# Performance work log

Measured on AMD Instinct MI355X. Metric: run time of the kernel, lower is better.

Reference implementation:

```python
import jax, jax.numpy as jnp
import numpy as np

EPS = 1e-5


def _lstm(x, W_ih, W_hh, b_ih, b_hh):
    # x: [B, T, in]; torch LSTM gate order i, f, g, o. Returns (last h, last c).
    def step(carry, xt):
        h, c = carry
        z = xt @ W_ih.T + h @ W_hh.T + (b_ih + b_hh)  # [B, 4H]
        i, f, g, o = jnp.split(z, 4, axis=-1)
        c = jax.nn.sigmoid(f) * c + jax.nn.sigmoid(i) * jnp.tanh(g)
        h = jax.nn.sigmoid(o) * jnp.tanh(c)
        return (h, c), None
    h0 = jnp.zeros((x.shape[0], W_hh.shape[1]), x.dtype)
    (h, c), _ = jax.lax.scan(step, (h0, h0), jnp.swapaxes(x, 0, 1))
    return h, c


def _bn_train(x, g, b):
    # BatchNorm1d in training mode: batch stats, biased variance.
    m = x.mean(axis=0)
    v = x.var(axis=0)
    return g * (x - m) * jax.lax.rsqrt(v + EPS) + b


def _forward(agent_traj, neighbours, aW_ih, aW_hh, ab_ih, ab_hh,
             nW_ih, nW_hh, nb_ih, nb_hh, dW_ih, dW_hh, db_ih, db_hh,
             pW, pb, rW, rb, m1W, m1b, g1, be1, m2W, m2b, g2, be2,
             i1W, i1b, ig1, ib1, i2W, i2b, ig2, ib2, segment_ids):
    B = agent_traj.shape[0]
    # relative distance: neighbour last position - owning agent's last position
    rel = neighbours[:, -1, :] - agent_traj[segment_ids, -1, :]          # [N, 2]
    agent_h, agent_c = _lstm(agent_traj, aW_ih, aW_hh, ab_ih, ab_hh)     # [B, 64]
    neigh_h, _ = _lstm(neighbours, nW_ih, nW_hh, nb_ih, nb_hh)           # [N, 64]
    rel_emb = rel @ rW.T + rb                                            # [N, 64]
    x = jnp.concatenate([neigh_h, rel_emb], axis=1)                      # [N, 128]
    x = _bn_train(jax.nn.relu(x @ m1W.T + m1b), g1, be1)                 # [N, 512]
    x = _bn_train(jax.nn.relu(x @ m2W.T + m2b), g2, be2)                 # [N, 1024]
    # per-sample max pooling over each sample's neighbours (zeros if none)
    pooled = jax.ops.segment_max(x, segment_ids, num_segments=B)         # [B, 1024]
    counts = jax.ops.segment_sum(jnp.ones((x.shape[0],), x.dtype), segment_ids, num_segments=B)
    pooled = jnp.where(counts[:, None] > 0, pooled, jnp.zeros((), x.dtype))
    d = jnp.concatenate([pooled, agent_h], axis=1)                       # [B, 1088]
    d = _bn_train(jax.nn.relu(d @ i1W.T + i1b), ig1, ib1)                # [B, 1024]
    d = _bn_train(jax.nn.relu(d @ i2W.T + i2b), ig2, ib2)                # [B, 64]

    def dec_step(carry, _):
        h, c = carry
        z = h @ dW_ih.T + h @ dW_hh.T + (db_ih + db_hh)
        i, f, g, o = jnp.split(z, 4, axis=-1)
        c = jax.nn.sigmoid(f) * c + jax.nn.sigmoid(i) * jnp.tanh(g)
        h = jax.nn.sigmoid(o) * jnp.tanh(c)
        return (h, c), h
    _, hs = jax.lax.scan(dec_step, (d, agent_c), None, length=30)        # [30, B, 64]
    pred = jnp.einsum('tbh,oh->bto', hs, pW) + pb                        # [B, 30, 2]
    return pred


def setup_inputs() -> dict:
    B, T, N, Tn, H = 2048, 20, 32768, 20, 64
    key = jax.random.key(0)
    ki = iter(jax.random.split(key, 40))
    def rn(shape, s=0.1):
        return jax.random.normal(next(ki), shape, dtype=jnp.float32) * s
    inp = dict(
        agent_traj=rn((B, T, 2), 1.0),
        neighbours=rn((N, Tn, 2), 1.0),
        aW_ih=rn((4 * H, 2)), aW_hh=rn((4 * H, H)), ab_ih=rn((4 * H,)), ab_hh=rn((4 * H,)),
        nW_ih=rn((4 * H, 2)), nW_hh=rn((4 * H, H)), nb_ih=rn((4 * H,)), nb_hh=rn((4 * H,)),
        dW_ih=rn((4 * H, H)), dW_hh=rn((4 * H, H)), db_ih=rn((4 * H,)), db_hh=rn((4 * H,)),
        pW=rn((2, H)), pb=rn((2,)),
        rW=rn((H, 2)), rb=rn((H,)),
        m1W=rn((512, 128)), m1b=rn((512,)),
        g1=jnp.ones((512,), jnp.float32), be1=jnp.zeros((512,), jnp.float32),
        m2W=rn((1024, 512)), m2b=rn((1024,)),
        g2=jnp.ones((1024,), jnp.float32), be2=jnp.zeros((1024,), jnp.float32),
        i1W=rn((1024, 1088)), i1b=rn((1024,)),
        ig1=jnp.ones((1024,), jnp.float32), ib1=jnp.zeros((1024,), jnp.float32),
        i2W=rn((H, 1024)), i2b=rn((H,)),
        ig2=jnp.ones((H,), jnp.float32), ib2=jnp.zeros((H,), jnp.float32),
        segment_ids=jnp.sort(jax.random.randint(next(ki), (N,), 0, B)).astype(jnp.int32),
    )
    return inp


def reference(agent_traj, neighbours, aW_ih, aW_hh, ab_ih, ab_hh,
              nW_ih, nW_hh, nb_ih, nb_hh, dW_ih, dW_hh, db_ih, db_hh,
              pW, pb, rW, rb, m1W, m1b, g1, be1, m2W, m2b, g2, be2,
              i1W, i1b, ig1, ib1, i2W, i2b, ig2, ib2, segment_ids):
    return _forward(agent_traj, neighbours, aW_ih, aW_hh, ab_ih, ab_hh,
                    nW_ih, nW_hh, nb_ih, nb_hh, dW_ih, dW_hh, db_ih, db_hh,
                    pW, pb, rW, rb, m1W, m1b, g1, be1, m2W, m2b, g2, be2,
                    i1W, i1b, ig1, ib1, i2W, i2b, ig2, ib2, segment_ids)
```

## Files before the change

kernel.cpp:

```cpp
#include <hip/hip_runtime.h>

#define EPS_BN 1e-5f

typedef __attribute__((ext_vector_type(8))) short short8;
typedef __attribute__((ext_vector_type(4))) float f32x4;

__device__ __forceinline__ float fast_rcp(float x) { return __builtin_amdgcn_rcpf(x); }
__device__ __forceinline__ float sigmoid_f(float x) { return fast_rcp(1.0f + __expf(-x)); }
__device__ __forceinline__ float tanh_f(float x) { return 1.0f - 2.0f * fast_rcp(__expf(2.0f * x) + 1.0f); }

__device__ __forceinline__ unsigned short f2bf(float f) {
    unsigned u = __float_as_uint(f);
    u += 0x7FFFu + ((u >> 16) & 1u);
    return (unsigned short)(u >> 16);
}
__device__ __forceinline__ unsigned pk_bf(float a, float b) {
    return (unsigned)f2bf(a) | ((unsigned)f2bf(b) << 16);
}
__device__ __forceinline__ float bf_hi(float f) {
    return __uint_as_float((unsigned)f2bf(f) << 16);
}
__device__ __forceinline__ float bf2f(unsigned short u) {
    return __uint_as_float((unsigned)u << 16);
}

union AFrag { short e[8]; short8 v; };
union BFrag { uint4 u; short8 v; };

__global__ __launch_bounds__(256, 2) void lstm_mfma(
    const float* __restrict__ xA,
    const float* __restrict__ aW_ih, const float* __restrict__ aW_hh,
    const float* __restrict__ ab_ih, const float* __restrict__ ab_hh,
    float* __restrict__ agent_h, float* __restrict__ agent_c,
    const float* __restrict__ xN,
    const float* __restrict__ nW_ih, const float* __restrict__ nW_hh,
    const float* __restrict__ nb_ih, const float* __restrict__ nb_hh,
    float* __restrict__ neigh_h,
    int nAgentBlk, int T)
{
    __shared__ unsigned h_ex[2][2][32 * 52];

    const bool isA = (blockIdx.x < (unsigned)nAgentBlk);
    const long blk = isA ? blockIdx.x : blockIdx.x - nAgentBlk;
    const float* __restrict__ x     = isA ? xA   : xN;
    const float* __restrict__ W_ih  = isA ? aW_ih : nW_ih;
    const float* __restrict__ W_hh  = isA ? aW_hh : nW_hh;
    const float* __restrict__ b_ih  = isA ? ab_ih : nb_ih;
    const float* __restrict__ b_hh  = isA ? ab_hh : nb_hh;
    float* __restrict__ h_out = isA ? agent_h : neigh_h;
    float* __restrict__ c_out = isA ? agent_c : nullptr;

    const int tid  = threadIdx.x;
    const int w    = tid >> 6;
    const int lane = tid & 63;
    const int s    = lane & 15;
    const int q    = lane >> 4;

    short8 ahi[4][3], alo[4][3];
#pragma unroll
    for (int gt = 0; gt < 4; ++gt) {
        const int n = gt * 64 + w * 16 + s;
#pragma unroll
        for (int kc = 0; kc < 2; ++kc) {
            const float* src = &W_hh[n * 64 + kc * 32 + q * 8];
            float4 v0 = *(const float4*)src;
            float4 v1 = *(const float4*)(src + 4);
            float v[8] = {v0.x, v0.y, v0.z, v0.w, v1.x, v1.y, v1.z, v1.w};
            AFrag a, b;
#pragma unroll
            for (int j = 0; j < 8; ++j) {
                a.e[j] = (short)f2bf(v[j]);
                b.e[j] = (short)f2bf(v[j] - bf_hi(v[j]));
            }
            ahi[gt][kc] = a.v;
            alo[gt][kc] = b.v;
        }
        AFrag a2, b2;
#pragma unroll
        for (int j = 0; j < 8; ++j) { a2.e[j] = 0; b2.e[j] = 0; }
        if (q == 0) {
            const float wi0 = W_ih[n * 2 + 0];
            const float wi1 = W_ih[n * 2 + 1];
            const float bs  = b_ih[n] + b_hh[n];
            a2.e[0] = (short)f2bf(wi0); b2.e[0] = (short)f2bf(wi0 - bf_hi(wi0));
            a2.e[1] = (short)f2bf(wi1); b2.e[1] = (short)f2bf(wi1 - bf_hi(wi1));
            a2.e[2] = (short)f2bf(bs);  b2.e[2] = (short)f2bf(bs  - bf_hi(bs));
        }
        ahi[gt][2] = a2.v;
        alo[gt][2] = b2.v;
    }

    for (int i = tid; i < 2 * 2 * 32 * 52; i += 256) (&h_ex[0][0][0])[i] = 0u;
    __syncthreads();
    if (tid < 32) {
        h_ex[0][0][tid * 52 + 33] = pk_bf(1.0f, 0.0f);
        h_ex[1][0][tid * 52 + 33] = pk_bf(1.0f, 0.0f);
        float2 xv = *(const float2*)&x[(blk * 32 + tid) * (long)(T * 2)];
        h_ex[0][0][tid * 52 + 32] = pk_bf(xv.x, xv.y);
        h_ex[0][1][tid * 52 + 32] = pk_bf(xv.x - bf_hi(xv.x), xv.y - bf_hi(xv.y));
    }
    __syncthreads();

    float creg[2][4] = {{0.f, 0.f, 0.f, 0.f}, {0.f, 0.f, 0.f, 0.f}};

    for (int t = 0; t < T; ++t) {
        const int rb = t & 1, wb = rb ^ 1;
        BFrag bhi[2][3], blo[2][3];
#pragma unroll
        for (int g = 0; g < 2; ++g)
#pragma unroll
        for (int kc = 0; kc < 3; ++kc) {
            const int off = (g * 16 + s) * 52 + kc * 16 + (q >> 1) * 8 + (q & 1) * 4;
            bhi[g][kc].u = *(const uint4*)&h_ex[rb][0][off];
            blo[g][kc].u = *(const uint4*)&h_ex[rb][1][off];
        }

        f32x4 acc[4][2];
#pragma unroll
        for (int gt = 0; gt < 4; ++gt) { acc[gt][0] = (f32x4)0.f; acc[gt][1] = (f32x4)0.f; }

#pragma unroll
        for (int kc = 0; kc < 3; ++kc) {
#pragma unroll
            for (int g = 0; g < 2; ++g) {
                const short8 bh = bhi[g][kc].v;
                const short8 bl = blo[g][kc].v;
#pragma unroll
                for (int gt = 0; gt < 4; ++gt) {
                    f32x4 a = acc[gt][g];
                    a = __builtin_amdgcn_mfma_f32_16x16x32_bf16(ahi[gt][kc], bh, a, 0, 0, 0);
                    a = __builtin_amdgcn_mfma_f32_16x16x32_bf16(ahi[gt][kc], bl, a, 0, 0, 0);
                    a = __builtin_amdgcn_mfma_f32_16x16x32_bf16(alo[gt][kc], bh, a, 0, 0, 0);
                    acc[gt][g] = a;
                }
            }
        }

#pragma unroll
        for (int g = 0; g < 2; ++g) {
            float hval[4];
#pragma unroll
            for (int r = 0; r < 4; ++r) {
                const float ei = __expf(-acc[0][g][r]);
                const float eg = __expf(2.0f * acc[2][g][r]);
                const float it = (eg - 1.0f) * fast_rcp((1.0f + ei) * (eg + 1.0f));
                const float sf = fast_rcp(1.0f + __expf(-acc[1][g][r]));
                const float c  = fmaf(sf, creg[g][r], it);
                creg[g][r] = c;
                const float eo = __expf(-acc[3][g][r]);
                const float ec = __expf(2.0f * c);
                hval[r] = (ec - 1.0f) * fast_rcp((1.0f + eo) * (ec + 1.0f));
            }
            {
                const int w0 = (g * 16 + s) * 52 + w * 8 + q * 2;
                h_ex[wb][0][w0]     = pk_bf(hval[0], hval[1]);
                h_ex[wb][0][w0 + 1] = pk_bf(hval[2], hval[3]);
                h_ex[wb][1][w0]     = pk_bf(hval[0] - bf_hi(hval[0]), hval[1] - bf_hi(hval[1]));
                h_ex[wb][1][w0 + 1] = pk_bf(hval[2] - bf_hi(hval[2]), hval[3] - bf_hi(hval[3]));
            }
            if (t == T - 1) {
                const long seq = blk * 32 + g * 16 + s;
                const int j0 = w * 16 + q * 4;
                *(float4*)&h_out[seq * 64 + j0] = make_float4(hval[0], hval[1], hval[2], hval[3]);
                if (c_out)
                    *(float4*)&c_out[seq * 64 + j0] =
                        make_float4(creg[g][0], creg[g][1], creg[g][2], creg[g][3]);
            }
        }
        if (tid < 32 && t + 1 < T) {
            float2 xv = *(const float2*)&x[(blk * 32 + tid) * (long)(T * 2) + (t + 1) * 2];
            h_ex[wb][0][tid * 52 + 32] = pk_bf(xv.x, xv.y);
            h_ex[wb][1][tid * 52 + 32] = pk_bf(xv.x - bf_hi(xv.x), xv.y - bf_hi(xv.y));
        }
        __syncthreads();
    }
}

__global__ __launch_bounds__(256) void build_x0(
    const float* __restrict__ neigh_h, const float* __restrict__ neighbours,
    const float* __restrict__ agent_traj, const int* __restrict__ seg,
    const float* __restrict__ rW, const float* __restrict__ rb,
    unsigned short* __restrict__ x0hi, unsigned short* __restrict__ x0lo, int T)
{
    const long n = (long)blockIdx.x * 2 + (threadIdx.x >> 7);
    const int j = threadIdx.x & 127;
    float v;
    if (j < 64) {
        v = neigh_h[n*64 + j];
    } else {
        const int o = j - 64;
        const int sid = seg[n];
        const float ra = neighbours[n*(long)(T*2) + (T-1)*2 + 0] - agent_traj[(long)sid*(T*2) + (T-1)*2 + 0];
        const float rbv= neighbours[n*(long)(T*2) + (T-1)*2 + 1] - agent_traj[(long)sid*(T*2) + (T-1)*2 + 1];
        v = fmaf(rW[o*2+0], ra, fmaf(rW[o*2+1], rbv, rb[o]));
    }
    x0hi[n*128 + j] = f2bf(v);
    x0lo[n*128 + j] = f2bf(v - bf_hi(v));
}

__global__ __launch_bounds__(64) void prep_wfrag(
    const float* __restrict__ W, const float* __restrict__ sc, int K,
    unsigned short* __restrict__ Whi, unsigned short* __restrict__ Wlo)
{
    const int nKc = K >> 5;
    const int blk = blockIdx.x;
    const int ti = blk / nKc, kc = blk - ti * nKc;
    const int l = threadIdx.x;
    const int n = ti * 16 + (l & 15);
    const int k0 = kc * 32 + (l >> 4) * 8;
    const long ob = ((long)blk * 64 + l) * 8;
#pragma unroll
    for (int j = 0; j < 8; ++j) {
        float v = W[(long)n * K + k0 + j];
        if (sc) v *= sc[k0 + j];
        Whi[ob + j] = f2bf(v);
        Wlo[ob + j] = f2bf(v - bf_hi(v));
    }
}

__global__ __launch_bounds__(64) void prep_bias(
    const float* __restrict__ W, const float* __restrict__ sh,
    const float* __restrict__ b, int K, float* __restrict__ bout)
{
    const int n = blockIdx.x;
    const int l = threadIdx.x;
    float s = 0.f;
    if (sh)
        for (int k = l; k < K; k += 64) s += sh[k] * W[(long)n * K + k];
#pragma unroll
    for (int m = 32; m >= 1; m >>= 1) s += __shfl_xor(s, m, 64);
    if (l == 0) bout[n] = b[n] + s;
}

__global__ __launch_bounds__(256, 2) void gemm_split(
    const unsigned short* __restrict__ Ahi,
    const unsigned short* __restrict__ Alo,
    const unsigned short* __restrict__ Whi,
    const unsigned short* __restrict__ Wlo,
    const float* __restrict__ bias,
    float* __restrict__ Yf,
    unsigned short* __restrict__ Yhi,
    unsigned short* __restrict__ Ylo,
    float* __restrict__ accum,
    const int* __restrict__ segp,
    float* __restrict__ poolmax,
    int M, int K, int O)
{
    __shared__ unsigned short As[2][2][128 * 56];
    __shared__ int segl[128];
    const int t = threadIdx.x;
    const int lane = t & 63;
    const int w = t >> 6;
    const int wm = w & 1, wn = w >> 1;

    const int nx = gridDim.x;
    const int flat = blockIdx.y * nx + blockIdx.x;
    const int grp = flat / (8 * nx);
    const int loc = flat - grp * (8 * nx);
    const int m0 = (grp * 8 + (loc & 7)) * 128;
    const int n0 = (loc >> 3) * 128;
    const int nKc = K >> 5;

    f32x4 acc[4][4];
#pragma unroll
    for (int mt = 0; mt < 4; ++mt)
#pragma unroll
    for (int nt = 0; nt < 4; ++nt) acc[mt][nt] = (f32x4)0.f;

    const long aoff = (long)(m0 + (t >> 1)) * K + (t & 1) * 16;
    const unsigned short* aph = Ahi + aoff;
    const unsigned short* apl = Alo + aoff;
    const int so = (t >> 1) * 56 + (t & 1) * 16;
    const int arow = wm * 64 + (lane & 15);
    const int acol = (lane >> 4) * 8;
    const long bt0 = (long)((n0 >> 4) + wn * 4);

    uint4 rah0, rah1, ral0, ral1;
    auto loadAreg = [&](int kc) {
        rah0 = *(const uint4*)(aph + kc * 32);
        rah1 = *(const uint4*)(aph + kc * 32 + 8);
        ral0 = *(const uint4*)(apl + kc * 32);
        ral1 = *(const uint4*)(apl + kc * 32 + 8);
    };
    auto storeAs = [&](int buf) {
        *(uint4*)&As[buf][0][so] = rah0; *(uint4*)&As[buf][0][so + 8] = rah1;
        *(uint4*)&As[buf][1][so] = ral0; *(uint4*)&As[buf][1][so + 8] = ral1;
    };
    auto loadB = [&](BFrag* bh, BFrag* bl, int kc) {
#pragma unroll
        for (int nt = 0; nt < 4; ++nt) {
            const long fb = ((bt0 + nt) * nKc + kc) * 512 + lane * 8;
            bh[nt].u = *(const uint4*)(Whi + fb);
            bl[nt].u = *(const uint4*)(Wlo + fb);
        }
    };
    auto compute = [&](int buf, BFrag* bh, BFrag* bl) {
        BFrag afh[4], afl[4];
#pragma unroll
        for (int mt = 0; mt < 4; ++mt) {
            afh[mt].u = *(const uint4*)&As[buf][0][(arow + mt * 16) * 56 + acol];
            afl[mt].u = *(const uint4*)&As[buf][1][(arow + mt * 16) * 56 + acol];
        }
#pragma unroll
        for (int nt = 0; nt < 4; ++nt)
#pragma unroll
        for (int mt = 0; mt < 4; ++mt) {
            f32x4 a = acc[mt][nt];
            a = __builtin_amdgcn_mfma_f32_16x16x32_bf16(afh[mt].v, bh[nt].v, a, 0, 0, 0);
            a = __builtin_amdgcn_mfma_f32_16x16x32_bf16(afh[mt].v, bl[nt].v, a, 0, 0, 0);
            a = __builtin_amdgcn_mfma_f32_16x16x32_bf16(afl[mt].v, bh[nt].v, a, 0, 0, 0);
            acc[mt][nt] = a;
        }
    };

    BFrag bh0[4], bl0[4], bh1[4], bl1[4];
    loadAreg(0);
    loadB(bh0, bl0, 0);
    storeAs(0);
    __syncthreads();
    for (int kc = 0; kc < nKc; kc += 2) {
        loadAreg(kc + 1);
        loadB(bh1, bl1, kc + 1);
        compute(0, bh0, bl0);
        storeAs(1);
        __syncthreads();
        if (kc + 2 < nKc) {
            loadAreg(kc + 2);
            loadB(bh0, bl0, kc + 2);
        }
        compute(1, bh1, bl1);
        if (kc + 2 < nKc) {
            storeAs(0);
            __syncthreads();
        }
    }

    int sid0 = 0, span = 0;
    bool useLds = false;
    float* pool = nullptr;
    if (segp) {
        __syncthreads();
        if (t < 128) segl[t] = segp[m0 + t];
        __syncthreads();
        sid0 = segl[0];
        span = segl[127] - sid0 + 1;
        pool = (float*)&As[0][0][0];
        useLds = (span <= 104);
        if (useLds) {
            for (int i = t; i < span * 132; i += 256) pool[i] = 0.f;
            __syncthreads();
        }
    }

    const int cn = lane & 15, cq = lane >> 4;
#pragma unroll
    for (int nt = 0; nt < 4; ++nt) {
        const int cl = wn * 64 + nt * 16 + cn;
        const int n = n0 + cl;
        const float bs = bias[n];
        float s = 0.f, ssq = 0.f;
#pragma unroll
        for (int mt = 0; mt < 4; ++mt) {
            const int mb = wm * 64 + mt * 16 + cq * 4;
            float vmax = 0.f; int sid = -1;
#pragma unroll
            for (int r = 0; r < 4; ++r) {
                const float v = fmaxf(acc[mt][nt][r] + bs, 0.f);
                s += v; ssq += v * v;
                if (segp) {
                    const int sr = segl[mb + r];
                    if (r == 0) { vmax = v; sid = sr; }
                    else if (sr == sid) { vmax = fmaxf(vmax, v); }
                    else {
                        if (vmax > 0.f) {
                            if (useLds)
                                atomicMax((int*)&pool[(sid - sid0) * 132 + cl], __float_as_int(vmax));
                            else
                                atomicMax((int*)&poolmax[(long)sid * O + n], __float_as_int(vmax));
                        }
                        sid = sr; vmax = v;
                    }
                } else if (Yf) {
                    Yf[(long)(m0 + mb + r) * O + n] = v;
                } else {
                    const long idx = (long)(m0 + mb + r) * O + n;
                    Yhi[idx] = f2bf(v);
                    Ylo[idx] = f2bf(v - bf_hi(v));
                }
            }
            if (segp && vmax > 0.f) {
                if (useLds)
                    atomicMax((int*)&pool[(sid - sid0) * 132 + cl], __float_as_int(vmax));
                else
                    atomicMax((int*)&poolmax[(long)sid * O + n], __float_as_int(vmax));
            }
        }
        if (accum) {
            s   += __shfl_xor(s, 16, 64);   ssq += __shfl_xor(ssq, 16, 64);
            s   += __shfl_xor(s, 32, 64);   ssq += __shfl_xor(ssq, 32, 64);
            if (cq == 0) {
                atomicAdd(&accum[n], s);
                atomicAdd(&accum[O + n], ssq);
            }
        }
    }

    if (segp && useLds) {
        __syncthreads();
        for (int e = t; e < span * 128; e += 256) {
            const int sl = e >> 7, c = e & 127;
            const float v = pool[sl * 132 + c];
            const long gi = (long)(sid0 + sl) * O + (n0 + c);
            if (sl == 0 || sl == span - 1) {
                if (v > 0.f) atomicMax((int*)&poolmax[gi], __float_as_int(v));
            } else {
                poolmax[gi] = v;
            }
        }
    }
}

__global__ __launch_bounds__(256) void colstats(
    const float* __restrict__ Y, int M, int O, int chunkRows,
    float* __restrict__ accum)
{
    const int c = blockIdx.x * 64 + (threadIdx.x & 63);
    const int rgrp = threadIdx.x >> 6;
    const int r0 = blockIdx.y * chunkRows;
    int rend = r0 + chunkRows; if (rend > M) rend = M;
    float s = 0.f, ss = 0.f;
    for (int r = r0 + rgrp; r < rend; r += 4) {
        const float v = Y[(long)r*O + c];
        s += v; ss += v*v;
    }
    __shared__ float l1[256], l2[256];
    l1[threadIdx.x] = s; l2[threadIdx.x] = ss;
    __syncthreads();
    if (threadIdx.x < 64) {
        const int c2 = blockIdx.x * 64 + threadIdx.x;
        s  = l1[threadIdx.x] + l1[threadIdx.x+64] + l1[threadIdx.x+128] + l1[threadIdx.x+192];
        ss = l2[threadIdx.x] + l2[threadIdx.x+64] + l2[threadIdx.x+128] + l2[threadIdx.x+192];
        atomicAdd(&accum[c2], s);
        atomicAdd(&accum[O + c2], ss);
    }
}

__global__ __launch_bounds__(256) void bn_finalize(
    const float* __restrict__ accum, const float* __restrict__ g,
    const float* __restrict__ be, int O, float invM,
    float* __restrict__ scale, float* __restrict__ shift)
{
    const int o = blockIdx.x * 256 + threadIdx.x;
    if (o < O) {
        const float mean = accum[o] * invM;
        const float var  = accum[O + o] * invM - mean * mean;
        const float sc   = g[o] * rsqrtf(var + EPS_BN);
        scale[o] = sc;
        shift[o] = be[o] - mean * sc;
    }
}

__global__ __launch_bounds__(256) void build_d0(
    const float* __restrict__ poolraw, const float* __restrict__ agent_h,
    const int* __restrict__ seg, int N,
    const float* __restrict__ sc2, const float* __restrict__ sh2,
    unsigned short* __restrict__ d0hi, unsigned short* __restrict__ d0lo)
{
    const int b = blockIdx.x;
    int l = 0, h = N;
    while (l < h) { const int mid = (l + h) >> 1; if (seg[mid] < b) l = mid + 1; else h = mid; }
    const bool nonempty = (l < N) && (seg[l] == b);
    for (int c = threadIdx.x; c < 1088; c += 256) {
        float v;
        if (c < 1024) {
            v = nonempty ? fmaf(sc2[c], poolraw[(long)b*1024 + c], sh2[c]) : 0.f;
        } else {
            v = agent_h[(long)b*64 + (c - 1024)];
        }
        d0hi[(long)b*1088 + c] = f2bf(v);
        d0lo[(long)b*1088 + c] = f2bf(v - bf_hi(v));
    }
}

__global__ __launch_bounds__(256) void gemm_i2_part(
    const float* __restrict__ A,
    const float* __restrict__ W,
    const float* __restrict__ ascale, const float* __restrict__ ashift,
    float* __restrict__ part, int M, int K, int kchunk)
{
    __shared__ float As[16][132];
    __shared__ float Bs[16][68];
    const int t = threadIdx.x;
    const int m0 = blockIdx.x * 128;
    const int ks = blockIdx.y;
    const int kbeg = ks * kchunk;
    const int kend = kbeg + kchunk;
    const int tm = (t & 15) * 8;
    const int tn = (t >> 4) * 4;
    const int ar = t >> 1;
    const int ac = (t & 1) * 8;
    const int br = t >> 2;
    const int bc = (t & 3) * 4;

    float acc[8][4];
#pragma unroll
    for (int i = 0; i < 8; ++i)
#pragma unroll
    for (int j = 0; j < 4; ++j) acc[i][j] = 0.f;

    for (int k0 = kbeg; k0 < kend; k0 += 16) {
        float4 a0 = *(const float4*)&A[(long)(m0+ar)*K + k0 + ac];
        float4 a1 = *(const float4*)&A[(long)(m0+ar)*K + k0 + ac + 4];
        float4 s0 = *(const float4*)&ascale[k0 + ac];
        float4 s1 = *(const float4*)&ascale[k0 + ac + 4];
        float4 h0 = *(const float4*)&ashift[k0 + ac];
        float4 h1 = *(const float4*)&ashift[k0 + ac + 4];
        a0.x = fmaf(a0.x, s0.x, h0.x); a0.y = fmaf(a0.y, s0.y, h0.y);
        a0.z = fmaf(a0.z, s0.z, h0.z); a0.w = fmaf(a0.w, s0.w, h0.w);
        a1.x = fmaf(a1.x, s1.x, h1.x); a1.y = fmaf(a1.y, s1.y, h1.y);
        a1.z = fmaf(a1.z, s1.z, h1.z); a1.w = fmaf(a1.w, s1.w, h1.w);
        float4 b0 = *(const float4*)&W[(long)br*K + k0 + bc];
        __syncthreads();
        As[ac+0][ar] = a0.x; As[ac+1][ar] = a0.y; As[ac+2][ar] = a0.z; As[ac+3][ar] = a0.w;
        As[ac+4][ar] = a1.x; As[ac+5][ar] = a1.y; As[ac+6][ar] = a1.z; As[ac+7][ar] = a1.w;
        Bs[bc+0][br] = b0.x; Bs[bc+1][br] = b0.y; Bs[bc+2][br] = b0.z; Bs[bc+3][br] = b0.w;
        __syncthreads();
#pragma unroll
        for (int kk = 0; kk < 16; ++kk) {
            float av[8], bv[4];
            *(float4*)&av[0] = *(const float4*)&As[kk][tm];
            *(float4*)&av[4] = *(const float4*)&As[kk][tm + 4];
            *(float4*)&bv[0] = *(const float4*)&Bs[kk][tn];
#pragma unroll
            for (int i = 0; i < 8; ++i)
#pragma unroll
            for (int j = 0; j < 4; ++j)
                acc[i][j] = fmaf(av[i], bv[j], acc[i][j]);
        }
    }

    float* po = part + (long)ks * M * 64;
#pragma unroll
    for (int i = 0; i < 8; ++i)
        *(float4*)&po[(long)(m0 + tm + i) * 64 + tn] = *(float4*)&acc[i][0];
}

__global__ __launch_bounds__(256) void i2_finish(
    const float* __restrict__ part, const float* __restrict__ bias,
    int M, int KS, float* __restrict__ t2)
{
    const long idx = (long)blockIdx.x * 256 + threadIdx.x;
    if (idx < (long)M * 64) {
        float s = 0.f;
        for (int ks = 0; ks < KS; ++ks) s += part[(long)ks * M * 64 + idx];
        t2[idx] = fmaxf(s + bias[idx & 63], 0.f);
    }
}

__global__ __launch_bounds__(256) void prep_dec(
    const float* __restrict__ dW_ih, const float* __restrict__ dW_hh,
    const float* __restrict__ db_ih, const float* __restrict__ db_hh,
    float* __restrict__ Wc, float* __restrict__ bc)
{
    const int idx = blockIdx.x * 256 + threadIdx.x;
    if (idx < 256*64) Wc[idx] = dW_ih[idx] + dW_hh[idx];
    else if (idx < 256*64 + 256) bc[idx - 256*64] = db_ih[idx - 256*64] + db_hh[idx - 256*64];
}

__global__ __launch_bounds__(256) void decoder_kernel(
    const float* __restrict__ t2, const float* __restrict__ sc4,
    const float* __restrict__ sh4, const float* __restrict__ agent_c,
    const float* __restrict__ Wc, const float* __restrict__ bc,
    const float* __restrict__ pW, const float* __restrict__ pb,
    float* __restrict__ pred )
{
    __shared__ float h_lds[2][64];
    __shared__ float zg_lds[2][64];
    __shared__ float zo_lds[2][64];
    const int t = threadIdx.x;
    const int lane = t & 63;
    const int wave = t >> 6;
    const int s = wave >> 1;
    const int role = wave & 1;
    const long seq = (long)blockIdx.x * 2 + s;

    const int r0 = role * 128 + lane;
    const int r1 = r0 + 64;
    float w0[64], w1[64];
#pragma unroll
    for (int k = 0; k < 64; k += 4) {
        float4 va = *(const float4*)&Wc[r0 * 64 + k];
        w0[k] = va.x; w0[k+1] = va.y; w0[k+2] = va.z; w0[k+3] = va.w;
        float4 vb = *(const float4*)&Wc[r1 * 64 + k];
        w1[k] = vb.x; w1[k+1] = vb.y; w1[k+2] = vb.z; w1[k+3] = vb.w;
    }
    const float bias0 = bc[r0];
    const float bias1 = bc[r1];
    const float pw0 = pW[lane], pw1 = pW[64 + lane];
    const float pb0 = pb[0], pb1 = pb[1];

    float c = agent_c[seq*64 + lane];
    if (role == 0)
        h_lds[s][lane] = fmaf(sc4[lane], t2[seq*64 + lane], sh4[lane]);
    __syncthreads();
    float hv = h_lds[s][lane];

    for (int step = 0; step < 30; ++step) {
        float z0 = bias0, z1 = bias1;
#pragma unroll
        for (int k = 0; k < 64; ++k) {
            float hk = __int_as_float(__builtin_amdgcn_readlane(__float_as_int(hv), k));
            z0 = fmaf(hk, w0[k], z0);
            z1 = fmaf(hk, w1[k], z1);
        }
        if (role == 1) { zg_lds[s][lane] = z0; zo_lds[s][lane] = z1; }
        __syncthreads();
        if (role == 0) {
            const float ig = sigmoid_f(z0);
            const float fg = sigmoid_f(z1);
            const float gg = tanh_f(zg_lds[s][lane]);
            const float og = sigmoid_f(zo_lds[s][lane]);
            c = fmaf(fg, c, ig * gg);
            h_lds[s][lane] = og * tanh_f(c);
        }
        __syncthreads();
        hv = h_lds[s][lane];
        if (role == 0) {
            float p0 = hv * pw0;
            float p1 = hv * pw1;
#pragma unroll
            for (int m = 32; m >= 1; m >>= 1) {
                p0 += __shfl_xor(p0, m, 64);
                p1 += __shfl_xor(p1, m, 64);
            }
            if (lane == 0) {
                pred[seq*60 + step*2 + 0] = p0 + pb0;
                pred[seq*60 + step*2 + 1] = p1 + pb1;
            }
        }
    }
}

extern "C" void kernel_launch(void* const* d_in, const int* in_sizes, int n_in,
                              void* d_out, int out_size, void* d_ws, size_t ws_size,
                              hipStream_t stream)
{
    const float* agent_traj = (const float*)d_in[0];
    const float* neighbours = (const float*)d_in[1];
    const float* aW_ih = (const float*)d_in[2];
    const float* aW_hh = (const float*)d_in[3];
    const float* ab_ih = (const float*)d_in[4];
    const float* ab_hh = (const float*)d_in[5];
    const float* nW_ih = (const float*)d_in[6];
    const float* nW_hh = (const float*)d_in[7];
    const float* nb_ih = (const float*)d_in[8];
    const float* nb_hh = (const float*)d_in[9];
    const float* dW_ih = (const float*)d_in[10];
    const float* dW_hh = (const float*)d_in[11];
    const float* db_ih = (const float*)d_in[12];
    const float* db_hh = (const float*)d_in[13];
    const float* pW = (const float*)d_in[14];
    const float* pb = (const float*)d_in[15];
    const float* rW = (const float*)d_in[16];
    const float* rb = (const float*)d_in[17];
    const float* m1W = (const float*)d_in[18];
    const float* m1b = (const float*)d_in[19];
    const float* g1  = (const float*)d_in[20];
    const float* be1 = (const float*)d_in[21];
    const float* m2W = (const float*)d_in[22];
    const float* m2b = (const float*)d_in[23];
    const float* g2  = (const float*)d_in[24];
    const float* be2 = (const float*)d_in[25];
    const float* i1W = (const float*)d_in[26];
    const float* i1b = (const float*)d_in[27];
    const float* ig1 = (const float*)d_in[28];
    const float* ib1 = (const float*)d_in[29];
    const float* i2W = (const float*)d_in[30];
    const float* i2b = (const float*)d_in[31];
    const float* ig2 = (const float*)d_in[32];
    const float* ib2 = (const float*)d_in[33];
    const int*   seg = (const int*)d_in[34];
    float* pred = (float*)d_out;

    const int B = 2048, T = 20, N = 32768;

    char* p = (char*)d_ws;
    auto alloc = [&](size_t bytes) -> char* {
        char* r = p; p += (bytes + 255) & ~(size_t)255; return r;
    };
    float* agent_h = (float*)alloc((size_t)B*64*4);
    float* agent_c = (float*)alloc((size_t)B*64*4);
    char* neigh_region = alloc((size_t)N*64*4);
    unsigned short* x0hi = (unsigned short*)alloc((size_t)N*128*2);
    unsigned short* x0lo = (unsigned short*)alloc((size_t)N*128*2);
    char* y1hi_region  = alloc((size_t)N*512*2);
    unsigned short* y1lo = (unsigned short*)alloc((size_t)N*512*2);
    float* poolraw = (float*)alloc((size_t)B*1024*4);
    float* accAll = (float*)alloc((size_t)(1024+2048+2048+128)*4);
    float* acc1 = accAll;
    float* acc2 = accAll + 1024;
    float* acc3 = accAll + 3072;
    float* acc4 = accAll + 5120;
    float* sc1 = (float*)alloc(512*4);  float* sh1 = (float*)alloc(512*4);
    float* sc2 = (float*)alloc(1024*4); float* sh2 = (float*)alloc(1024*4);
    float* sc3 = (float*)alloc(1024*4); float* sh3 = (float*)alloc(1024*4);
    float* sc4 = (float*)alloc(64*4);   float* sh4 = (float*)alloc(64*4);
    float* Wc = (float*)alloc(256*64*4);
    float* bc = (float*)alloc(256*4);
    unsigned short* W1hi = (unsigned short*)alloc((size_t)512*128*2);
    unsigned short* W1lo = (unsigned short*)alloc((size_t)512*128*2);
    unsigned short* W2hi = (unsigned short*)alloc((size_t)1024*512*2);
    unsigned short* W2lo = (unsigned short*)alloc((size_t)1024*512*2);
    unsigned short* Wi1hi = (unsigned short*)alloc((size_t)1024*1088*2);
    unsigned short* Wi1lo = (unsigned short*)alloc((size_t)1024*1088*2);
    float* b1f = (float*)alloc(512*4);
    float* b2f = (float*)alloc(1024*4);
    float* bi1f = (float*)alloc(1024*4);
    float* i2part = (float*)alloc((size_t)8*B*64*4);

    float* neigh_h = (float*)neigh_region;
    float* t1      = (float*)neigh_region;
    unsigned short* y1hi = (unsigned short*)y1hi_region;
    unsigned short* d0hi = (unsigned short*)y1hi_region;
    unsigned short* d0lo = d0hi + (size_t)B*1088;
    float* t2 = (float*)(y1hi_region + (size_t)2*B*1088*2);

    hipMemsetAsync(accAll, 0, (1024+2048+2048+128)*sizeof(float), stream);
    hipMemsetAsync(poolraw, 0, (size_t)B*1024*4, stream);

    prep_wfrag<<<(512/16)*(128/32), 64, 0, stream>>>(m1W, nullptr, 128, W1hi, W1lo);
    prep_bias<<<512, 64, 0, stream>>>(m1W, nullptr, m1b, 128, b1f);
    prep_wfrag<<<(1024/16)*(1088/32), 64, 0, stream>>>(i1W, nullptr, 1088, Wi1hi, Wi1lo);
    prep_bias<<<1024, 64, 0, stream>>>(i1W, nullptr, i1b, 1088, bi1f);
    prep_dec<<<65, 256, 0, stream>>>(dW_ih, dW_hh, db_ih, db_hh, Wc, bc);

    lstm_mfma<<<B/32 + N/32, 256, 0, stream>>>(
        agent_traj, aW_ih, aW_hh, ab_ih, ab_hh, agent_h, agent_c,
        neighbours, nW_ih, nW_hh, nb_ih, nb_hh, neigh_h,
        B/32, T);
    build_x0<<<N/2, 256, 0, stream>>>(neigh_h, neighbours, agent_traj, seg, rW, rb,
                                      x0hi, x0lo, T);

    gemm_split<<<dim3(512/128, N/128), 256, 0, stream>>>(
        x0hi, x0lo, W1hi, W1lo, b1f, nullptr, y1hi, y1lo, acc1,
        nullptr, nullptr, N, 128, 512);
    bn_finalize<<<2, 256, 0, stream>>>(acc1, g1, be1, 512, 1.0f/N, sc1, sh1);

    prep_wfrag<<<(1024/16)*(512/32), 64, 0, stream>>>(m2W, sc1, 512, W2hi, W2lo);
    prep_bias<<<1024, 64, 0, stream>>>(m2W, sh1, m2b, 512, b2f);

    gemm_split<<<dim3(1024/128, N/128), 256, 0, stream>>>(
        y1hi, y1lo, W2hi, W2lo, b2f, nullptr, nullptr, nullptr, acc2,
        seg, poolraw, N, 512, 1024);
    bn_finalize<<<4, 256, 0, stream>>>(acc2, g2, be2, 1024, 1.0f/N, sc2, sh2);

    build_d0<<<B, 256, 0, stream>>>(poolraw, agent_h, seg, N, sc2, sh2, d0hi, d0lo);

    gemm_split<<<dim3(1024/128, B/128), 256, 0, stream>>>(
        d0hi, d0lo, Wi1hi, Wi1lo, bi1f, t1, nullptr, nullptr, acc3,
        nullptr, nullptr, B, 1088, 1024);
    bn_finalize<<<4, 256, 0, stream>>>(acc3, ig1, ib1, 1024, 1.0f/B, sc3, sh3);

    gemm_i2_part<<<dim3(B/128, 8), 256, 0, stream>>>(t1, i2W, sc3, sh3, i2part,
                                                     B, 1024, 128);
    i2_finish<<<(B*64)/256, 256, 0, stream>>>(i2part, i2b, B, 8, t2);
    colstats<<<dim3(1, 8), 256, 0, stream>>>(t2, B, 64, 256, acc4);
    bn_finalize<<<1, 256, 0, stream>>>(acc4, ig2, ib2, 64, 1.0f/B, sc4, sh4);

    decoder_kernel<<<B/2, 256, 0, stream>>>(t2, sc4, sh4, agent_c, Wc, bc, pW, pb, pred);
}
```

Baseline: 608.7 us.

## Stage GEMM A tiles via direct global-to-LDS loads with XOR swizzle

Replaces the register round-trip for the A operand (global load into VGPRs, then LDS store) with global_load_lds direct-to-LDS transfers. An XOR-swizzled unpadded layout replaces the padded rows to avoid bank conflicts. This drops the explicit LDS store step and shrinks LDS use. The smaller LDS buffer also lowers the span threshold for the in-LDS segment max pooling, so more tiles fall back to the global pooling path. The loop still waits for the async LDS writes only at __syncthreads, which may not be a sufficient wait (vmcnt) for the direct loads.

```diff
diff --git a/kernel.cpp b/kernel.cpp
--- a/kernel.cpp
+++ b/kernel.cpp
@@ -22,6 +22,13 @@
 }
 __device__ __forceinline__ float bf2f(unsigned short u) {
     return __uint_as_float((unsigned)u << 16);
+}
+
+__device__ __forceinline__ void gload16(const unsigned short* g, unsigned short* l) {
+    __builtin_amdgcn_global_load_lds(
+        (const __attribute__((address_space(1))) unsigned int*)g,
+        (__attribute__((address_space(3))) unsigned int*)l,
+        16, 0, 0);
 }
 
 union AFrag { short e[8]; short8 v; };
@@ -246,7 +253,7 @@
     float* __restrict__ poolmax,
     int M, int K, int O)
 {
-    __shared__ unsigned short As[2][2][128 * 56];
+    __shared__ unsigned short As[2][2][128 * 32];
     __shared__ int segl[128];
     const int t = threadIdx.x;
     const int lane = t & 63;
@@ -267,25 +274,28 @@
 #pragma unroll
     for (int nt = 0; nt < 4; ++nt) acc[mt][nt] = (f32x4)0.f;
 
-    const long aoff = (long)(m0 + (t >> 1)) * K + (t & 1) * 16;
-    const unsigned short* aph = Ahi + aoff;
-    const unsigned short* apl = Alo + aoff;
-    const int so = (t >> 1) * 56 + (t & 1) * 16;
+    const int rloc0 = w * 32 + (lane >> 2);
+    const int rloc1 = rloc0 + 16;
+    const int sd = lane & 3;
+    const unsigned short* gsrc[2][2];
+    gsrc[0][0] = Ahi + (long)(m0 + rloc0) * K + (sd ^ ((rloc0 >> 1) & 3)) * 8;
+    gsrc[0][1] = Ahi + (long)(m0 + rloc1) * K + (sd ^ ((rloc1 >> 1) & 3)) * 8;
+    gsrc[1][0] = Alo + (long)(m0 + rloc0) * K + (sd ^ ((rloc0 >> 1) & 3)) * 8;
+    gsrc[1][1] = Alo + (long)(m0 + rloc1) * K + (sd ^ ((rloc1 >> 1) & 3)) * 8;
+
+    auto stageA = [&](int buf, int kc) {
+#pragma unroll
+        for (int pp = 0; pp < 2; ++pp)
+#pragma unroll
+        for (int cc = 0; cc < 2; ++cc)
+            gload16(gsrc[pp][cc] + kc * 32,
+                    &As[buf][pp][(w * 32 + cc * 16) * 32]);
+    };
+
+    const int s2 = ((lane >> 4) ^ ((lane >> 1) & 3)) * 8;
     const int arow = wm * 64 + (lane & 15);
-    const int acol = (lane >> 4) * 8;
     const long bt0 = (long)((n0 >> 4) + wn * 4);
 
-    uint4 rah0, rah1, ral0, ral1;
-    auto loadAreg = [&](int kc) {
-        rah0 = *(const uint4*)(aph + kc * 32);
-        rah1 = *(const uint4*)(aph + kc * 32 + 8);
-        ral0 = *(const uint4*)(apl + kc * 32);
-        ral1 = *(const uint4*)(apl + kc * 32 + 8);
-    };
-    auto storeAs = [&](int buf) {
-        *(uint4*)&As[buf][0][so] = rah0; *(uint4*)&As[buf][0][so + 8] = rah1;
-        *(uint4*)&As[buf][1][so] = ral0; *(uint4*)&As[buf][1][so + 8] = ral1;
-    };
     auto loadB = [&](BFrag* bh, BFrag* bl, int kc) {
 #pragma unroll
         for (int nt = 0; nt < 4; ++nt) {
@@ -298,8 +308,8 @@
         BFrag afh[4], afl[4];
 #pragma unroll
         for (int mt = 0; mt < 4; ++mt) {
-            afh[mt].u = *(const uint4*)&As[buf][0][(arow + mt * 16) * 56 + acol];
-            afl[mt].u = *(const uint4*)&As[buf][1][(arow + mt * 16) * 56 + acol];
+            afh[mt].u = *(const uint4*)&As[buf][0][(arow + mt * 16) * 32 + s2];
+            afl[mt].u = *(const uint4*)&As[buf][1][(arow + mt * 16) * 32 + s2];
         }
 #pragma unroll
         for (int nt = 0; nt < 4; ++nt)
@@ -314,25 +324,20 @@
     };
 
     BFrag bh0[4], bl0[4], bh1[4], bl1[4];
-    loadAreg(0);
+    stageA(0, 0);
     loadB(bh0, bl0, 0);
-    storeAs(0);
     __syncthreads();
     for (int kc = 0; kc < nKc; kc += 2) {
-        loadAreg(kc + 1);
+        stageA(1, kc + 1);
         loadB(bh1, bl1, kc + 1);
         compute(0, bh0, bl0);
-        storeAs(1);
         __syncthreads();
         if (kc + 2 < nKc) {
-            loadAreg(kc + 2);
+            stageA(0, kc + 2);
             loadB(bh0, bl0, kc + 2);
         }
         compute(1, bh1, bl1);
-        if (kc + 2 < nKc) {
-            storeAs(0);
-            __syncthreads();
-        }
+        if (kc + 2 < nKc) __syncthreads();
     }
 
     int sid0 = 0, span = 0;
@@ -345,7 +350,7 @@
         sid0 = segl[0];
         span = segl[127] - sid0 + 1;
         pool = (float*)&As[0][0][0];
-        useLds = (span <= 104);
+        useLds = (span <= 60);
         if (useLds) {
             for (int i = t; i < span * 132; i += 256) pool[i] = 0.f;
             __syncthreads();
```

Result: no change. 610.8 us (+0.3%).
